# Kernel tuning notes

Hardware: AMD Instinct MI355X
Metric: run time of the kernel (lower is better)

Reference implementation:

```python
import jax, jax.numpy as jnp
import numpy as np

NUM_MODELS = 64
IN_F, HID, OUT_F = 6, 64, 3
SQRT_K = float(np.sqrt(1.0 / NUM_MODELS))


def _uniform(key, shape):
    return jax.random.uniform(key, shape, dtype=jnp.float32, minval=-SQRT_K, maxval=SQRT_K)


def setup_inputs() -> dict:
    key = jax.random.key(0)
    keys = jax.random.split(key, 11)
    B = 131072
    inp = {"inputs": jax.random.normal(keys[0], (B, IN_F), dtype=jnp.float32)}
    # 5 MultiModelLinear layers: 6->64, 64->64 x3, 64->3
    dims = [(IN_F, HID), (HID, HID), (HID, HID), (HID, HID), (HID, OUT_F)]
    for i, (fin, fout) in enumerate(dims):
        inp[f"w{i}"] = _uniform(keys[1 + 2 * i], (NUM_MODELS, fout, fin))
        inp[f"b{i}"] = _uniform(keys[2 + 2 * i], (NUM_MODELS, fout))
    return inp


def _mm_linear(x, W, b, idx):
    # Per-sample weight gather then batched matvec: (B,out,in) @ (B,in) -> (B,out)
    return jnp.einsum("boi,bi->bo", W[idx], x) + b[idx]


def reference(inputs, w0, b0, w1, b1, w2, b2, w3, b3, w4, b4):
    B = inputs.shape[0]
    two_pi = 2.0 * jnp.pi
    # 'angle' selection mode
    angles = jnp.arctan2(inputs[:, 2], inputs[:, 0])
    angles = jnp.mod(angles + two_pi, two_pi) / two_pi * NUM_MODELS
    selection_indices = jnp.floor(angles).astype(jnp.int32)
    selection_logits = jnp.ones((B, NUM_MODELS), dtype=inputs.dtype)
    selection_probabilities = jax.nn.softmax(selection_logits, axis=1)

    x = inputs
    for (W, b) in ((w0, b0), (w1, b1), (w2, b2), (w3, b3)):
        x = jax.nn.relu(_mm_linear(x, W, b, selection_indices))
    x = _mm_linear(x, w4, b4, selection_indices)  # (B, 3)

    top_outputs = x[:, None, :]  # num_top_outputs == 1
    model_output = x
    return (model_output, top_outputs, selection_indices,
            selection_logits, selection_probabilities)
```

## Files before the change

### kernel.cpp

```cpp
#include <hip/hip_runtime.h>
#include <hip/hip_bf16.h>

#define B_ROWS 131072
#define TWO_PI_F 6.28318530717958647692f

#define OUT_TOP    393216
#define OUT_SEL    786432
#define OUT_LOGITS 917504
#define OUT_PROBS  9306112

#define WS_SEL    0
#define WS_BLK    131072
#define WS_ROWS   163840
#define WS_GMOD   299008
#define NGRP_MAX  2112

typedef float vfloat4 __attribute__((ext_vector_type(4)));

__device__ __forceinline__ float rl(float v, int lane) {
    return __int_as_float(__builtin_amdgcn_readlane(__float_as_int(v), lane));
}

__global__ __launch_bounds__(256) void k_prep(const float* __restrict__ in,
                                              float* __restrict__ out,
                                              int* __restrict__ sel,
                                              int* __restrict__ blkCnt) {
    __shared__ int hist[64];
    const int tid = threadIdx.x, bid = blockIdx.x;
    if (tid < 64) hist[tid] = 0;
    __syncthreads();

    const int r = bid * 256 + tid;
    const float xx = in[r * 6 + 0];
    const float zz = in[r * 6 + 2];
    float a = atan2f(zz, xx);
    a = fmodf(a + TWO_PI_F, TWO_PI_F);
    const float t = a / TWO_PI_F * 64.0f;
    int s = (int)floorf(t);
    s = s < 0 ? 0 : (s > 63 ? 63 : s);
    sel[r] = s;
    out[OUT_SEL + r] = (float)s;
    atomicAdd(&hist[s], 1);

    {
        vfloat4* lg = (vfloat4*)(out + OUT_LOGITS);
        vfloat4* pb = (vfloat4*)(out + OUT_PROBS);
        const vfloat4 ones = {1.f, 1.f, 1.f, 1.f};
        const vfloat4 pr = {0.015625f, 0.015625f, 0.015625f, 0.015625f};
#pragma unroll
        for (int k = 0; k < 16; ++k) {
            __builtin_nontemporal_store(ones, lg + r + k * B_ROWS);
            __builtin_nontemporal_store(pr, pb + r + k * B_ROWS);
        }
    }

    __syncthreads();
    if (tid < 64) blkCnt[bid * 64 + tid] = hist[tid];
}

__global__ void k_scan(int* __restrict__ blkCnt, int* __restrict__ gmodel) {
    const int m = threadIdx.x;
    int tot = 0;
    for (int b = 0; b < 512; ++b) tot += blkCnt[b * 64 + m];
    const int grp = (tot + 63) >> 6;

    __shared__ int shP[64], shG[64];
    shP[m] = grp << 6;
    shG[m] = grp;
    __syncthreads();
    int offP = 0, offG = 0;
    for (int j = 0; j < m; ++j) { offP += shP[j]; offG += shG[j]; }

    int run = offP;
    for (int b = 0; b < 512; ++b) {
        const int c = blkCnt[b * 64 + m];
        blkCnt[b * 64 + m] = run;
        run += c;
    }
    for (int i = 0; i < grp; ++i) gmodel[offG + i] = m;
}

__global__ __launch_bounds__(256) void k_scatter(const int* __restrict__ sel,
                                                 const int* __restrict__ blkBase,
                                                 int* __restrict__ rowsArr) {
    __shared__ int cur[64];
    const int tid = threadIdx.x, bid = blockIdx.x;
    if (tid < 64) cur[tid] = blkBase[bid * 64 + tid];
    __syncthreads();
    const int r = bid * 256 + tid;
    const int s = sel[r];
    const int pos = atomicAdd(&cur[s], 1);
    rowsArr[pos] = r;
}

__global__ __launch_bounds__(64, 2) void k_mlp_rl(
    const float* __restrict__ in,
    const float* __restrict__ w0, const float* __restrict__ b0,
    const float* __restrict__ w1, const float* __restrict__ b1,
    const float* __restrict__ w2, const float* __restrict__ b2,
    const float* __restrict__ w3, const float* __restrict__ b3,
    const float* __restrict__ w4, const float* __restrict__ b4,
    const int* __restrict__ gmodel, const int* __restrict__ rowsArr,
    float* __restrict__ out) {
    const int m = gmodel[blockIdx.x];
    if (m < 0) return;
    const int lane = threadIdx.x;
    __shared__ float stage[64 * 66];
    float* myst = stage + lane * 66;

    const int row = rowsArr[blockIdx.x * 64 + lane];
    const bool valid = row >= 0;
    const int r = valid ? row : 0;

    const float* xin = in + r * 6;
    const float x0 = xin[0], x1 = xin[1], x2 = xin[2];
    const float x3 = xin[3], x4 = xin[4], x5 = xin[5];

    {
        const float* W0 = w0 + m * 384 + lane * 6;
        const float wa0 = W0[0], wa1 = W0[1], wa2 = W0[2];
        const float wa3 = W0[3], wa4 = W0[4], wa5 = W0[5];
        const float bv = b0[m * 64 + lane];
#pragma unroll 2
        for (int o = 0; o < 64; ++o) {
            float a = rl(bv, o);
            a = fmaf(rl(wa0, o), x0, a);
            a = fmaf(rl(wa1, o), x1, a);
            a = fmaf(rl(wa2, o), x2, a);
            a = fmaf(rl(wa3, o), x3, a);
            a = fmaf(rl(wa4, o), x4, a);
            a = fmaf(rl(wa5, o), x5, a);
            myst[o] = fmaxf(a, 0.f);
        }
    }

#pragma unroll 1
    for (int l = 0; l < 3; ++l) {
        const float* Wl = (l == 0 ? w1 : l == 1 ? w2 : w3) + m * 4096;
        const float* blp = (l == 0 ? b1 : l == 1 ? b2 : b3) + m * 64;
        float4 wq[16];
        const float4* Wr = (const float4*)(Wl + lane * 64);
#pragma unroll
        for (int q = 0; q < 16; ++q) wq[q] = Wr[q];
        const float bv = blp[lane];

        float h[64];
#pragma unroll
        for (int j = 0; j < 32; ++j) {
            const float2 t = *(const float2*)(myst + 2 * j);
            h[2 * j] = t.x;
            h[2 * j + 1] = t.y;
        }
#pragma unroll 2
        for (int o = 0; o < 64; ++o) {
            float a = rl(bv, o);
#pragma unroll
            for (int q = 0; q < 16; ++q) {
                const float4 wv = wq[q];
                a = fmaf(rl(wv.x, o), h[4 * q + 0], a);
                a = fmaf(rl(wv.y, o), h[4 * q + 1], a);
                a = fmaf(rl(wv.z, o), h[4 * q + 2], a);
                a = fmaf(rl(wv.w, o), h[4 * q + 3], a);
            }
            myst[o] = fmaxf(a, 0.f);
        }
    }

    {
        float h[64];
#pragma unroll
        for (int j = 0; j < 32; ++j) {
            const float2 t = *(const float2*)(myst + 2 * j);
            h[2 * j] = t.x;
            h[2 * j + 1] = t.y;
        }
        const float c0 = w4[m * 192 + lane];
        const float c1 = w4[m * 192 + 64 + lane];
        const float c2 = w4[m * 192 + 128 + lane];
        const float b4v = (lane < 3) ? b4[m * 3 + lane] : 0.f;
        float y0 = rl(b4v, 0), y1 = rl(b4v, 1), y2 = rl(b4v, 2);
#pragma unroll
        for (int k = 0; k < 64; ++k) {
            y0 = fmaf(rl(c0, k), h[k], y0);
            y1 = fmaf(rl(c1, k), h[k], y1);
            y2 = fmaf(rl(c2, k), h[k], y2);
        }
        if (valid) {
            out[row * 3 + 0] = y0;
            out[row * 3 + 1] = y1;
            out[row * 3 + 2] = y2;
            float* top = out + OUT_TOP;
            top[row * 3 + 0] = y0;
            top[row * 3 + 1] = y1;
            top[row * 3 + 2] = y2;
        }
    }
}

extern "C" void kernel_launch(void* const* d_in, const int* in_sizes, int n_in,
                              void* d_out, int out_size, void* d_ws, size_t ws_size,
                              hipStream_t stream) {
    const float* in = (const float*)d_in[0];
    const float* w0 = (const float*)d_in[1];
    const float* b0 = (const float*)d_in[2];
    const float* w1 = (const float*)d_in[3];
    const float* b1 = (const float*)d_in[4];
    const float* w2 = (const float*)d_in[5];
    const float* b2 = (const float*)d_in[6];
    const float* w3 = (const float*)d_in[7];
    const float* b3 = (const float*)d_in[8];
    const float* w4 = (const float*)d_in[9];
    const float* b4 = (const float*)d_in[10];
    float* out = (float*)d_out;
    int* ws = (int*)d_ws;

    int* sel = ws + WS_SEL;
    int* blkCnt = ws + WS_BLK;
    int* rowsArr = ws + WS_ROWS;
    int* gmodel = ws + WS_GMOD;

    (void)hipMemsetAsync(rowsArr, 0xFF, (135168 + NGRP_MAX) * sizeof(int), stream);

    k_prep<<<512, 256, 0, stream>>>(in, out, sel, blkCnt);
    k_scan<<<1, 64, 0, stream>>>(blkCnt, gmodel);
    k_scatter<<<512, 256, 0, stream>>>(sel, blkCnt, rowsArr);
    k_mlp_rl<<<NGRP_MAX, 64, 0, stream>>>(in, w0, b0, w1, b1, w2, b2, w3, b3,
                                          w4, b4, gmodel, rowsArr, out);
}
```

Measured before the change: 342.8 us.

## Parallelize model scan across blocks and use uniform weight loads in MLP

New measurement: 400.6 us. +16.9%, slower.

```diff
diff --git a/kernel.cpp b/kernel.cpp
--- a/kernel.cpp
+++ b/kernel.cpp
@@ -13,18 +13,16 @@
 #define WS_BLK    131072
 #define WS_ROWS   163840
 #define WS_GMOD   299008
+#define WS_TOT    301120
 #define NGRP_MAX  2112
 
 typedef float vfloat4 __attribute__((ext_vector_type(4)));
-
-__device__ __forceinline__ float rl(float v, int lane) {
-    return __int_as_float(__builtin_amdgcn_readlane(__float_as_int(v), lane));
-}
 
 __global__ __launch_bounds__(256) void k_prep(const float* __restrict__ in,
                                               float* __restrict__ out,
                                               int* __restrict__ sel,
-                                              int* __restrict__ blkCnt) {
+                                              int* __restrict__ blkCnt,
+                                              int* __restrict__ tot) {
     __shared__ int hist[64];
     const int tid = threadIdx.x, bid = blockIdx.x;
     if (tid < 64) hist[tid] = 0;
@@ -55,29 +53,48 @@
     }
 
     __syncthreads();
-    if (tid < 64) blkCnt[bid * 64 + tid] = hist[tid];
-}
-
-__global__ void k_scan(int* __restrict__ blkCnt, int* __restrict__ gmodel) {
-    const int m = threadIdx.x;
-    int tot = 0;
-    for (int b = 0; b < 512; ++b) tot += blkCnt[b * 64 + m];
-    const int grp = (tot + 63) >> 6;
-
-    __shared__ int shP[64], shG[64];
-    shP[m] = grp << 6;
-    shG[m] = grp;
-    __syncthreads();
-    int offP = 0, offG = 0;
-    for (int j = 0; j < m; ++j) { offP += shP[j]; offG += shG[j]; }
-
-    int run = offP;
-    for (int b = 0; b < 512; ++b) {
-        const int c = blkCnt[b * 64 + m];
-        blkCnt[b * 64 + m] = run;
-        run += c;
-    }
-    for (int i = 0; i < grp; ++i) gmodel[offG + i] = m;
+    if (tid < 64) {
+        blkCnt[bid * 64 + tid] = hist[tid];
+        atomicAdd(&tot[tid], hist[tid]);
+    }
+}
+
+__global__ __launch_bounds__(64) void k_scanwrite(int* __restrict__ blkCnt,
+                                                  const int* __restrict__ tot,
+                                                  int* __restrict__ gmodel) {
+    const int lane = threadIdx.x;
+    const int bm = blockIdx.x;
+
+    const int t = tot[lane];
+    const int grp = (t + 63) >> 6;
+    int inc = grp;
+#pragma unroll
+    for (int off = 1; off < 64; off <<= 1) {
+        const int n = __shfl_up(inc, off, 64);
+        if (lane >= off) inc += n;
+    }
+    const int exg = inc - grp;
+    const int offG = __shfl(exg, bm, 64);
+    const int myGrp = __shfl(grp, bm, 64);
+    const int padBase = offG << 6;
+
+    for (int i = lane; i < myGrp; i += 64) gmodel[offG + i] = bm;
+
+    int c[8];
+    int s = 0;
+#pragma unroll
+    for (int j = 0; j < 8; ++j) c[j] = blkCnt[(lane * 8 + j) * 64 + bm];
+#pragma unroll
+    for (int j = 0; j < 8; ++j) { const int v = c[j]; c[j] = s; s += v; }
+    int incs = s;
+#pragma unroll
+    for (int off = 1; off < 64; off <<= 1) {
+        const int n = __shfl_up(incs, off, 64);
+        if (lane >= off) incs += n;
+    }
+    const int exs = incs - s;
+#pragma unroll
+    for (int j = 0; j < 8; ++j) blkCnt[(lane * 8 + j) * 64 + bm] = padBase + exs + c[j];
 }
 
 __global__ __launch_bounds__(256) void k_scatter(const int* __restrict__ sel,
@@ -93,7 +110,7 @@
     rowsArr[pos] = r;
 }
 
-__global__ __launch_bounds__(64, 2) void k_mlp_rl(
+__global__ __launch_bounds__(64, 2) void k_mlp(
     const float* __restrict__ in,
     const float* __restrict__ w0, const float* __restrict__ b0,
     const float* __restrict__ w1, const float* __restrict__ b1,
@@ -116,83 +133,78 @@
     const float x0 = xin[0], x1 = xin[1], x2 = xin[2];
     const float x3 = xin[3], x4 = xin[4], x5 = xin[5];
 
+    float h[64];
+
     {
-        const float* W0 = w0 + m * 384 + lane * 6;
-        const float wa0 = W0[0], wa1 = W0[1], wa2 = W0[2];
-        const float wa3 = W0[3], wa4 = W0[4], wa5 = W0[5];
-        const float bv = b0[m * 64 + lane];
-#pragma unroll 2
+        const float* W0 = w0 + m * 384;
+        const float* B0 = b0 + m * 64;
+#pragma unroll
         for (int o = 0; o < 64; ++o) {
-            float a = rl(bv, o);
-            a = fmaf(rl(wa0, o), x0, a);
-            a = fmaf(rl(wa1, o), x1, a);
-            a = fmaf(rl(wa2, o), x2, a);
-            a = fmaf(rl(wa3, o), x3, a);
-            a = fmaf(rl(wa4, o), x4, a);
-            a = fmaf(rl(wa5, o), x5, a);
-            myst[o] = fmaxf(a, 0.f);
+            const float2 wa = *(const float2*)(W0 + o * 6);
+            const float2 wb = *(const float2*)(W0 + o * 6 + 2);
+            const float2 wc = *(const float2*)(W0 + o * 6 + 4);
+            float a = B0[o];
+            a = fmaf(wa.x, x0, a);
+            a = fmaf(wa.y, x1, a);
+            a = fmaf(wb.x, x2, a);
+            a = fmaf(wb.y, x3, a);
+            a = fmaf(wc.x, x4, a);
+            a = fmaf(wc.y, x5, a);
+            h[o] = fmaxf(a, 0.f);
         }
     }
 
 #pragma unroll 1
     for (int l = 0; l < 3; ++l) {
         const float* Wl = (l == 0 ? w1 : l == 1 ? w2 : w3) + m * 4096;
-        const float* blp = (l == 0 ? b1 : l == 1 ? b2 : b3) + m * 64;
-        float4 wq[16];
-        const float4* Wr = (const float4*)(Wl + lane * 64);
-#pragma unroll
-        for (int q = 0; q < 16; ++q) wq[q] = Wr[q];
-        const float bv = blp[lane];
-
-        float h[64];
-#pragma unroll
-        for (int j = 0; j < 32; ++j) {
-            const float2 t = *(const float2*)(myst + 2 * j);
-            h[2 * j] = t.x;
-            h[2 * j + 1] = t.y;
-        }
-#pragma unroll 2
+        const float* Bl = (l == 0 ? b1 : l == 1 ? b2 : b3) + m * 64;
+#pragma unroll 4
         for (int o = 0; o < 64; ++o) {
-            float a = rl(bv, o);
+            float a = Bl[o];
+            const float4* wr = (const float4*)(Wl + o * 64);
 #pragma unroll
             for (int q = 0; q < 16; ++q) {
-                const float4 wv = wq[q];
-                a = fmaf(rl(wv.x, o), h[4 * q + 0], a);
-                a = fmaf(rl(wv.y, o), h[4 * q + 1], a);
-                a = fmaf(rl(wv.z, o), h[4 * q + 2], a);
-                a = fmaf(rl(wv.w, o), h[4 * q + 3], a);
+                const float4 wv = wr[q];
+                a = fmaf(wv.x, h[4 * q + 0], a);
+                a = fmaf(wv.y, h[4 * q + 1], a);
+                a = fmaf(wv.z, h[4 * q + 2], a);
+                a = fmaf(wv.w, h[4 * q + 3], a);
             }
             myst[o] = fmaxf(a, 0.f);
         }
+#pragma unroll
+        for (int j = 0; j < 32; ++j) {
+            const float2 t2 = *(const float2*)(myst + 2 * j);
+            h[2 * j] = t2.x;
+            h[2 * j + 1] = t2.y;
+        }
     }
 
     {
-        float h[64];
-#pragma unroll
-        for (int j = 0; j < 32; ++j) {
-            const float2 t = *(const float2*)(myst + 2 * j);
-            h[2 * j] = t.x;
-            h[2 * j + 1] = t.y;
-        }
-        const float c0 = w4[m * 192 + lane];
-        const float c1 = w4[m * 192 + 64 + lane];
-        const float c2 = w4[m * 192 + 128 + lane];
-        const float b4v = (lane < 3) ? b4[m * 3 + lane] : 0.f;
-        float y0 = rl(b4v, 0), y1 = rl(b4v, 1), y2 = rl(b4v, 2);
-#pragma unroll
-        for (int k = 0; k < 64; ++k) {
-            y0 = fmaf(rl(c0, k), h[k], y0);
-            y1 = fmaf(rl(c1, k), h[k], y1);
-            y2 = fmaf(rl(c2, k), h[k], y2);
+        const float* W4 = w4 + m * 192;
+        float y[3];
+#pragma unroll
+        for (int c = 0; c < 3; ++c) {
+            float a = b4[m * 3 + c];
+            const float4* wr = (const float4*)(W4 + c * 64);
+#pragma unroll
+            for (int q = 0; q < 16; ++q) {
+                const float4 wv = wr[q];
+                a = fmaf(wv.x, h[4 * q + 0], a);
+                a = fmaf(wv.y, h[4 * q + 1], a);
+                a = fmaf(wv.z, h[4 * q + 2], a);
+                a = fmaf(wv.w, h[4 * q + 3], a);
+            }
+            y[c] = a;
         }
         if (valid) {
-            out[row * 3 + 0] = y0;
-            out[row * 3 + 1] = y1;
-            out[row * 3 + 2] = y2;
+            out[row * 3 + 0] = y[0];
+            out[row * 3 + 1] = y[1];
+            out[row * 3 + 2] = y[2];
             float* top = out + OUT_TOP;
-            top[row * 3 + 0] = y0;
-            top[row * 3 + 1] = y1;
-            top[row * 3 + 2] = y2;
+            top[row * 3 + 0] = y[0];
+            top[row * 3 + 1] = y[1];
+            top[row * 3 + 2] = y[2];
         }
     }
 }
@@ -218,12 +230,14 @@
     int* blkCnt = ws + WS_BLK;
     int* rowsArr = ws + WS_ROWS;
     int* gmodel = ws + WS_GMOD;
+    int* tot = ws + WS_TOT;
 
     (void)hipMemsetAsync(rowsArr, 0xFF, (135168 + NGRP_MAX) * sizeof(int), stream);
-
-    k_prep<<<512, 256, 0, stream>>>(in, out, sel, blkCnt);
-    k_scan<<<1, 64, 0, stream>>>(blkCnt, gmodel);
+    (void)hipMemsetAsync(tot, 0, 64 * sizeof(int), stream);
+
+    k_prep<<<512, 256, 0, stream>>>(in, out, sel, blkCnt, tot);
+    k_scanwrite<<<64, 64, 0, stream>>>(blkCnt, tot, gmodel);
     k_scatter<<<512, 256, 0, stream>>>(sel, blkCnt, rowsArr);
-    k_mlp_rl<<<NGRP_MAX, 64, 0, stream>>>(in, w0, b0, w1, b1, w2, b2, w3, b3,
-                                          w4, b4, gmodel, rowsArr, out);
-}
+    k_mlp<<<NGRP_MAX, 64, 0, stream>>>(in, w0, b0, w1, b1, w2, b2, w3, b3,
+                                       w4, b4, gmodel, rowsArr, out);
+}
```
